# Kernel tuning notes

Measured on AMD Instinct MI355X. Metric: run time of the kernel, lower is better.

## Reference

```python
import jax, jax.numpy as jnp
import numpy as np
from jax import lax
from jax.scipy.stats import norm

K = 2            # top-k
NUM_EXPERTS = 4
NOISE_EPS = 0.01
LOSS_COEF = 0.01


def conv3x3(x, w):
    # x: [B,Cin,H,W], w: [Cout,Cin,3,3] -> [B,Cout,H,W]
    return lax.conv_general_dilated(x, w, (1, 1), 'SAME',
                                    dimension_numbers=('NCHW', 'OIHW', 'NCHW'))


def setup_inputs() -> dict:
    key = jax.random.key(0)
    ks = jax.random.split(key, 16)
    B, C, H, W = 16, 3, 256, 256
    FC = 2 * C                      # freq channels = 6
    HID = 64
    D = H * W * C                   # flattened gating dim = 196608
    f32 = jnp.float32
    inp = {
        'x':   jax.random.normal(ks[0], (B, C, H, W), f32),
        'ref': jax.random.normal(ks[1], (B, C, H, W), f32),
        'noise': jax.random.normal(ks[2], (B, NUM_EXPERTS), f32),
        'mod_w1': (jax.random.normal(ks[3], (FC, 2 * FC), f32) * 0.1),
        'mod_b1': jnp.zeros((FC,), f32),
        'mod_w2': (jax.random.normal(ks[4], (FC, FC), f32) * 0.1),
        'mod_b2': jnp.zeros((FC,), f32),
        'enh_w': (jax.random.normal(ks[5], (FC, FC), f32) * 0.1),
        'enh_b': jnp.zeros((FC,), f32),
        'fre_prompt': (jax.random.normal(ks[6], (FC, H, W // 2 + 1), f32) * 0.1),
        'w_gate':  (jax.random.normal(ks[7], (D, NUM_EXPERTS), f32) * 0.002),
        'w_noise': (jax.random.normal(ks[8], (D, NUM_EXPERTS), f32) * 0.002),
        'ew1': (jax.random.normal(ks[9],  (NUM_EXPERTS, HID, C, 3, 3), f32) * 0.05),
        'eb1': jnp.zeros((NUM_EXPERTS, HID), f32),
        'ew2': (jax.random.normal(ks[10], (NUM_EXPERTS, 1, HID, 3, 3), f32) * 0.05),
        'eb2': jnp.zeros((NUM_EXPERTS, 1), f32),
    }
    return inp


def _cv_squared(v):
    # torch .var() is unbiased (ddof=1)
    return jnp.var(v, ddof=1) / (jnp.mean(v) ** 2 + 1e-10)


def _forward(x, ref, noise, mod_w1, mod_b1, mod_w2, mod_b2, enh_w, enh_b,
             fre_prompt, w_gate, w_noise, ew1, eb1, ew2, eb2):
    B, C, H, W = x.shape

    # ---- frequency_prompt(ref) ----
    fft = jnp.fft.rfft2(ref, norm='ortho')                    # [B,C,H,W//2+1]
    freq = jnp.concatenate([fft.real, fft.imag], axis=1)      # [B,2C,H,Wf]
    # Adaptive avg/max pool to (H, W//2+1) are identities at native size
    pooled = jnp.concatenate([freq, freq], axis=1)            # [B,4C,H,Wf]
    m = jnp.einsum('oi,bihw->bohw', mod_w1, pooled) + mod_b1[:, None, None]
    m = jax.nn.relu(m)
    m = jnp.einsum('oi,bihw->bohw', mod_w2, m) + mod_b2[:, None, None]
    enh = m * fre_prompt[None]                                # [B,2C,H,Wf]
    enh = jax.nn.relu(jnp.einsum('oi,bihw->bohw', enh_w, enh) + enh_b[:, None, None])
    re, im = jnp.split(enh, 2, axis=1)
    spatial = jnp.fft.irfft2(re + 1j * im, s=(H, W), norm='ortho')  # [B,C,H,W]
    prompt = jax.nn.softmax(spatial.mean(axis=(2, 3), keepdims=True), axis=1)  # [B,C,1,1]

    # ---- noisy top-k gating ----
    x_ds = (x * prompt + x).reshape(B, -1)                    # [B, H*W*C]
    clean_logits = x_ds @ w_gate                              # [B,E]
    noise_stddev = jax.nn.softplus(x_ds @ w_noise) + NOISE_EPS
    noisy_logits = clean_logits + noise * noise_stddev
    top_vals, top_idx = lax.top_k(noisy_logits, K + 1)        # sorted desc, [B,K+1]
    tk_gates = jax.nn.softmax(top_vals[:, :K], axis=1)        # [B,K]
    gates = jnp.zeros_like(noisy_logits).at[
        jnp.arange(B)[:, None], top_idx[:, :K]].set(tk_gates)  # [B,E]

    # load = prob each expert's noisy logit lands in top-k
    thr_in = top_vals[:, K:K + 1]
    thr_out = top_vals[:, K - 1:K]
    is_in = noisy_logits > thr_in
    prob = jnp.where(is_in,
                     norm.cdf((clean_logits - thr_in) / noise_stddev),
                     norm.cdf((clean_logits - thr_out) / noise_stddev))
    load = prob.sum(0)
    importance = gates.sum(0)
    loss = (_cv_squared(importance) + _cv_squared(load)) * LOSS_COEF

    # ---- expert dispatch/combine (== weighted sum; gates are 0 off top-k) ----
    y = jnp.zeros((B, ew2.shape[1], H, W), x.dtype)
    for e in range(NUM_EXPERTS):
        h = jax.nn.relu(conv3x3(x, ew1[e]) + eb1[e][None, :, None, None])
        o = conv3x3(h, ew2[e]) + eb2[e][None, :, None, None]
        y = y + gates[:, e][:, None, None, None] * o
    return y, loss


def reference(x, ref, noise, mod_w1, mod_b1, mod_w2, mod_b2, enh_w, enh_b,
              fre_prompt, w_gate, w_noise, ew1, eb1, ew2, eb2):
    return _forward(x, ref, noise, mod_w1, mod_b1, mod_w2, mod_b2, enh_w, enh_b,
                    fre_prompt, w_gate, w_noise, ew1, eb1, ew2, eb2)
```

## Files before the change

kernel.cpp:

```cpp
#include <hip/hip_runtime.h>
#include <hip/hip_bf16.h>
#include <math.h>

#define WS_GATE 192
#define WS_GNP  256
#define WS_W1F  25088
#define WS_W2F  29184

typedef float    float4v __attribute__((ext_vector_type(4)));
typedef short    short8v __attribute__((ext_vector_type(8)));
typedef _Float16 half8v  __attribute__((ext_vector_type(8)));

union Q4 { uint4 q; short8v s; half8v h; };

__device__ __forceinline__ unsigned short bf16b(float f) {
    unsigned u = __builtin_bit_cast(unsigned, f);
    u = (u + 0x7FFFu + ((u >> 16) & 1u)) >> 16;
    return (unsigned short)u;
}

__device__ __forceinline__ unsigned pkbf16(float a, float b) {
#if __has_builtin(__builtin_amdgcn_cvt_pk_bf16_f32)
    return __builtin_bit_cast(unsigned, __builtin_amdgcn_cvt_pk_bf16_f32(a, b));
#else
    return (unsigned)bf16b(a) | ((unsigned)bf16b(b) << 16);
#endif
}

__device__ __forceinline__ unsigned pkf16(float a, float b) {
#if __has_builtin(__builtin_amdgcn_cvt_pkrtz)
    return __builtin_bit_cast(unsigned, __builtin_amdgcn_cvt_pkrtz(a, b));
#else
    union { _Float16 h[2]; unsigned u; } p;
    p.h[0] = (_Float16)a; p.h[1] = (_Float16)b;
    return p.u;
#endif
}

__global__ void k_aux(const float* __restrict__ ref, const float* __restrict__ x,
                      const float* __restrict__ wg,  const float* __restrict__ wn,
                      const float* __restrict__ ew1, const float* __restrict__ ew2,
                      float* __restrict__ ws) {
    __shared__ float sh[4][16][8];
    int blk = blockIdx.x, t = threadIdx.x;

    if (blk < 192) {
        int bc = blk >> 2, chunk = blk & 3;
        const float4* p4 = (const float4*)(ref + (size_t)bc*65536 + (size_t)chunk*16384);
        float acc = 0.f;
        #pragma unroll
        for (int i = 0; i < 16; ++i) { float4 v = p4[i*256 + t]; acc += v.x + v.y + v.z + v.w; }
        #pragma unroll
        for (int m = 1; m <= 32; m <<= 1) acc += __shfl_xor(acc, m);
        if ((t & 63) == 0) sh[0][0][t >> 6] = acc;
        __syncthreads();
        if (t == 0) ws[bc*4 + chunk] = sh[0][0][0] + sh[0][0][1] + sh[0][0][2] + sh[0][0][3];
        return;
    }
    if (blk < 384) {
        int r = blk - 192;
        int c = r >> 6, chunk = r & 63;
        int lane = t & 63, wv = t >> 6;
        int hw0 = chunk*1024 + t*4;
        const float4* wg4 = (const float4*)wg;
        const float4* wn4 = (const float4*)wn;
        const float4* x4  = (const float4*)x;
        float4 G[4], Nw[4];
        #pragma unroll
        for (int i = 0; i < 4; ++i) {
            G[i]  = wg4[c*65536 + hw0 + i];
            Nw[i] = wn4[c*65536 + hw0 + i];
        }
        for (int b = 0; b < 16; ++b) {
            float4 xv = x4[(b*3 + c)*16384 + chunk*256 + t];
            float xs[4] = {xv.x, xv.y, xv.z, xv.w};
            float aG[4] = {0,0,0,0}, aN[4] = {0,0,0,0};
            #pragma unroll
            for (int i = 0; i < 4; ++i) {
                aG[0] += xs[i]*G[i].x;  aG[1] += xs[i]*G[i].y;
                aG[2] += xs[i]*G[i].z;  aG[3] += xs[i]*G[i].w;
                aN[0] += xs[i]*Nw[i].x; aN[1] += xs[i]*Nw[i].y;
                aN[2] += xs[i]*Nw[i].z; aN[3] += xs[i]*Nw[i].w;
            }
            #pragma unroll
            for (int m = 1; m <= 32; m <<= 1) {
                #pragma unroll
                for (int e = 0; e < 4; ++e) {
                    aG[e] += __shfl_xor(aG[e], m);
                    aN[e] += __shfl_xor(aN[e], m);
                }
            }
            if (lane == 0) {
                #pragma unroll
                for (int e = 0; e < 4; ++e) { sh[wv][b][e] = aG[e]; sh[wv][b][4+e] = aN[e]; }
            }
        }
        __syncthreads();
        if (t < 128) {
            int b = t >> 3, s = t & 7;
            float v = sh[0][b][s] + sh[1][b][s] + sh[2][b][s] + sh[3][b][s];
            ws[WS_GNP + ((size_t)(c*64 + chunk)*16 + b)*8 + s] = v;
        }
        return;
    }
    uint4* w1f = (uint4*)(ws + WS_W1F);
    for (int i = t; i < 1024; i += 256) {
        int mm = i & 15, r = i >> 4, qq = r & 3, r2 = r >> 2, f = r2 & 3, e = r2 >> 2;
        const float* w1 = ew1 + e*1728 + (f*16 + mm)*27 + qq*8;
        int navail = 27 - qq*8;
        float v[8];
        #pragma unroll
        for (int j = 0; j < 8; ++j) v[j] = (j < navail) ? w1[j] : 0.f;
        uint4 q;
        q.x = pkbf16(v[0], v[1]); q.y = pkbf16(v[2], v[3]);
        q.z = pkbf16(v[4], v[5]); q.w = pkbf16(v[6], v[7]);
        w1f[i] = q;
    }
    uint4* w2f = (uint4*)(ws + WS_W2F);
    for (int i = t; i < 512; i += 256) {
        int qq = i & 3, r = i >> 2, ks = r & 1, r2 = r >> 1, mm = r2 & 15, e = r2 >> 4;
        uint4 q = make_uint4(0, 0, 0, 0);
        if (mm < 9) {
            float v[8];
            #pragma unroll
            for (int j = 0; j < 8; ++j) v[j] = ew2[e*576 + (ks*32 + qq*8 + j)*9 + mm];
            q.x = pkf16(v[0], v[1]); q.y = pkf16(v[2], v[3]);
            q.z = pkf16(v[4], v[5]); q.w = pkf16(v[6], v[7]);
        }
        w2f[i] = q;
    }
}

__global__ void k_gating(const float* __restrict__ noise,
                         const float* __restrict__ mw1, const float* __restrict__ mb1,
                         const float* __restrict__ mw2, const float* __restrict__ mb2,
                         const float* __restrict__ enw, const float* __restrict__ enb,
                         const float* __restrict__ fp,
                         float* __restrict__ ws, float* __restrict__ out) {
    __shared__ float GN2[48*8];
    __shared__ float gL[16][4], pL[16][4], cvs[2];
    int t = threadIdx.x;
    #pragma unroll
    for (int u = 0; u < 3; ++u) {
        int idx = t*3 + u;
        int bc = idx >> 3, s = idx & 7;
        int b = bc / 3, c = bc - b*3;
        float v = 0.f;
        for (int ch = 0; ch < 64; ++ch)
            v += ws[WS_GNP + ((size_t)(c*64 + ch)*16 + b)*8 + s];
        GN2[bc*8 + s] = v;
    }
    __syncthreads();
    if (t < 16) {
        int b = t;
        float sc[3];
        for (int c = 0; c < 3; ++c) {
            int bc = b*3 + c;
            sc[c] = (ws[bc*4] + ws[bc*4+1] + ws[bc*4+2] + ws[bc*4+3]) * (1.f/256.f);
        }
        float pooled[12];
        for (int i = 0; i < 12; ++i) { int r = i % 6; pooled[i] = (r < 3) ? sc[r] : 0.f; }
        float m1[6];
        for (int o = 0; o < 6; ++o) {
            float a = mb1[o];
            for (int i = 0; i < 12; ++i) a += mw1[o*12 + i] * pooled[i];
            m1[o] = fmaxf(a, 0.f);
        }
        float m2[6];
        for (int o = 0; o < 6; ++o) {
            float a = mb2[o];
            for (int i = 0; i < 6; ++i) a += mw2[o*6 + i] * m1[i];
            m2[o] = a * fp[(size_t)o * 33024];
        }
        float dc[3];
        for (int o = 0; o < 3; ++o) {
            float a = enb[o];
            for (int i = 0; i < 6; ++i) a += enw[o*6 + i] * m2[i];
            dc[o] = fmaxf(a, 0.f) * (1.f/256.f);
        }
        float mx = fmaxf(dc[0], fmaxf(dc[1], dc[2]));
        float e0 = expf(dc[0]-mx), e1 = expf(dc[1]-mx), e2 = expf(dc[2]-mx);
        float inv = 1.f / (e0 + e1 + e2);
        float pc[3] = { e0*inv + 1.f, e1*inv + 1.f, e2*inv + 1.f };
        float cl[4], sg[4], nz[4];
        for (int e = 0; e < 4; ++e) {
            float a = 0.f, nr = 0.f;
            for (int c = 0; c < 3; ++c) {
                a  += pc[c] * GN2[(b*3 + c)*8 + e];
                nr += pc[c] * GN2[(b*3 + c)*8 + 4 + e];
            }
            cl[e] = a;
            float sp = (nr > 20.f) ? nr : log1pf(expf(nr));
            sg[e] = sp + 0.01f;
            nz[e] = a + noise[b*4 + e] * sg[e];
        }
        int i0 = 0; float v0 = nz[0];
        for (int e = 1; e < 4; ++e) if (nz[e] > v0) { v0 = nz[e]; i0 = e; }
        int i1 = -1; float v1 = -3.4e38f;
        for (int e = 0; e < 4; ++e) if (e != i0 && nz[e] > v1) { v1 = nz[e]; i1 = e; }
        float v2 = -3.4e38f;
        for (int e = 0; e < 4; ++e) if (e != i0 && e != i1 && nz[e] > v2) v2 = nz[e];
        float ex = expf(v1 - v0), den = 1.f + ex;
        float gate[4] = {0.f, 0.f, 0.f, 0.f};
        gate[i0] = 1.f/den; gate[i1] = ex/den;
        for (int e = 0; e < 4; ++e) {
            ws[WS_GATE + b*4 + e] = gate[e];
            gL[b][e] = gate[e];
            float thr = (nz[e] > v2) ? v2 : v1;
            pL[b][e] = 0.5f * (1.f + erff((cl[e] - thr) / sg[e] * 0.70710678118f));
        }
    }
    __syncthreads();
    if (t < 2) {
        float v[4];
        for (int e = 0; e < 4; ++e) {
            float s = 0.f;
            for (int b = 0; b < 16; ++b) s += (t == 0) ? gL[b][e] : pL[b][e];
            v[e] = s;
        }
        float mean = 0.25f * (v[0] + v[1] + v[2] + v[3]);
        float var = 0.f;
        for (int e = 0; e < 4; ++e) { float d = v[e] - mean; var += d*d; }
        var *= (1.f/3.f);
        cvs[t] = var / (mean*mean + 1e-10f);
    }
    __syncthreads();
    if (t == 0) out[1048576] = (cvs[0] + cvs[1]) * 0.01f;
}

__global__ __launch_bounds__(256, 3)
void k_experts(const float* __restrict__ x,  const float* __restrict__ eb1,
               const float* __restrict__ eb2, const float* __restrict__ ws,
               float* __restrict__ out) {
    __shared__ __align__(16) uint4 s_hid[324*8];
    __shared__ __align__(16) char  s_mix[5904];
    float*    in_s = (float*)s_mix;
    _Float16* s_T  = (_Float16*)s_mix;

    int t = threadIdx.x;
    int b = blockIdx.x >> 8, tile = blockIdx.x & 255;
    int ty0 = (tile >> 4) * 16, tx0 = (tile & 15) * 16;
    const float* xb = x + (size_t)b * 196608;

    for (int i = t; i < 1200; i += 256) {
        int ci = i / 400, r = i - ci*400, iy = r / 20, ix = r - iy*20;
        int gy = ty0 - 2 + iy, gx = tx0 - 2 + ix;
        float v = 0.f;
        if ((unsigned)gy < 256u && (unsigned)gx < 256u) v = xb[ci*65536 + gy*256 + gx];
        in_s[i] = v;
    }
    __syncthreads();

    int lane = t & 63, wv = t >> 6;
    int qq = lane >> 4, mm = lane & 15;
    int oy = t >> 4, ox = t & 15;

    int offj[8];
    #pragma unroll
    for (int j = 0; j < 8; ++j) {
        int k = qq*8 + j;
        if (k < 27) { int ci = k/9, r = k - ci*9, kh = r/3, kw = r - kh*3;
                      offj[j] = ci*400 + kh*20 + kw; }
        else offj[j] = -1;
    }

    Q4 bfr[6];
    #pragma unroll
    for (int i = 0; i < 6; ++i) {
        int gidx = wv + i*4;
        if (gidx >= 21) break;
        int p = gidx*16 + mm;
        int py = p/18, px = p - py*18;
        int base = (p < 324) ? (py*20 + px) : 0;
        float v[8];
        #pragma unroll
        for (int j = 0; j < 8; ++j)
            v[j] = (offj[j] >= 0) ? in_s[base + offj[j]] : 0.f;
        bfr[i].q.x = pkbf16(v[0], v[1]); bfr[i].q.y = pkbf16(v[2], v[3]);
        bfr[i].q.z = pkbf16(v[4], v[5]); bfr[i].q.w = pkbf16(v[6], v[7]);
    }

    bool interior = (ty0 > 0) && (ty0 < 240) && (tx0 > 0) && (tx0 < 240);
    const float4 gates = *(const float4*)(ws + WS_GATE + b*4);
    float gv[4] = {gates.x, gates.y, gates.z, gates.w};
    const uint4* w1f = (const uint4*)(ws + WS_W1F);
    const uint4* w2f = (const uint4*)(ws + WS_W2F);
    float accY = 0.f;

    for (int e = 0; e < 4; ++e) {
        float g = gv[e];
        if (g == 0.f) continue;

        Q4 bw0, bw1;
        bw0.q = w2f[((e*16 + mm)*2 + 0)*4 + qq];
        bw1.q = w2f[((e*16 + mm)*2 + 1)*4 + qq];

        Q4 af[4];
        float4v cinit[4];
        #pragma unroll
        for (int f = 0; f < 4; ++f) {
            af[f].q = w1f[((e*4 + f)*4 + qq)*16 + mm];
            float4 bb = *(const float4*)(eb1 + e*64 + f*16 + qq*4);
            cinit[f] = (float4v){bb.x, bb.y, bb.z, bb.w};
        }

        #pragma unroll
        for (int i = 0; i < 6; ++i) {
            int gidx = wv + i*4;
            if (gidx >= 21) break;
            int p = gidx*16 + mm;
            bool valid = p < 324;
            float msk = 1.f;
            if (!interior) {
                int py = p/18, px = p - py*18;
                int gy = ty0 - 1 + py, gx = tx0 - 1 + px;
                msk = (((unsigned)gy < 256u) && ((unsigned)gx < 256u)) ? 1.f : 0.f;
            }
            #pragma unroll
            for (int f = 0; f < 4; ++f) {
                float4v d = __builtin_amdgcn_mfma_f32_16x16x32_bf16(
                    af[f].s, bfr[i].s, cinit[f], 0, 0, 0);
                if (valid) {
                    float h0 = fmaxf(d[0], 0.f);
                    float h1 = fmaxf(d[1], 0.f);
                    float h2 = fmaxf(d[2], 0.f);
                    float h3 = fmaxf(d[3], 0.f);
                    if (!interior) { h0 *= msk; h1 *= msk; h2 *= msk; h3 *= msk; }
                    uint2 pk = make_uint2(pkf16(h0, h1), pkf16(h2, h3));
                    int ch0 = f*16 + qq*4;
                    int hchunk = ch0 >> 3, hsel = (ch0 >> 2) & 1;
                    ((uint2*)&s_hid[p*8 + ((hchunk + p) & 7)])[hsel] = pk;
                }
            }
        }
        __syncthreads();

        for (int gi = wv; gi < 21; gi += 4) {
            int base = gi*16; if (base > 308) base = 308;
            int p = base + mm;
            Q4 a0, a1;
            a0.q = s_hid[p*8 + ((qq + p) & 7)];
            a1.q = s_hid[p*8 + ((4 + qq + p) & 7)];
            float4v d = __builtin_amdgcn_mfma_f32_16x16x32_f16(
                a0.h, bw0.h, (float4v){0.f,0.f,0.f,0.f}, 0, 0, 0);
            d = __builtin_amdgcn_mfma_f32_16x16x32_f16(a1.h, bw1.h, d, 0, 0, 0);
            if (mm < 9) {
                *(uint2*)&s_T[mm*328 + base + qq*4] =
                    make_uint2(pkf16(d[0], d[1]), pkf16(d[2], d[3]));
            }
        }
        __syncthreads();

        float oacc = 0.f;
        #pragma unroll
        for (int kh = 0; kh < 3; ++kh) {
            #pragma unroll
            for (int kw = 0; kw < 3; ++kw)
                oacc += (float)s_T[(kh*3 + kw)*328 + (oy + kh)*18 + ox + kw];
        }
        accY += g * (oacc + eb2[e]);
    }
    out[(size_t)b*65536 + (ty0 + oy)*256 + tx0 + ox] = accY;
}

extern "C" void kernel_launch(void* const* d_in, const int* in_sizes, int n_in,
                              void* d_out, int out_size, void* d_ws, size_t ws_size,
                              hipStream_t stream) {
    (void)in_sizes; (void)n_in; (void)out_size; (void)ws_size;
    const float* x     = (const float*)d_in[0];
    const float* ref   = (const float*)d_in[1];
    const float* noise = (const float*)d_in[2];
    const float* mw1   = (const float*)d_in[3];
    const float* mb1   = (const float*)d_in[4];
    const float* mw2   = (const float*)d_in[5];
    const float* mb2   = (const float*)d_in[6];
    const float* enw   = (const float*)d_in[7];
    const float* enb   = (const float*)d_in[8];
    const float* fp    = (const float*)d_in[9];
    const float* wg    = (const float*)d_in[10];
    const float* wn    = (const float*)d_in[11];
    const float* ew1   = (const float*)d_in[12];
    const float* eb1   = (const float*)d_in[13];
    const float* ew2   = (const float*)d_in[14];
    const float* eb2   = (const float*)d_in[15];
    float* out = (float*)d_out;
    float* ws  = (float*)d_ws;

    k_aux    <<<385, 256, 0, stream>>>(ref, x, wg, wn, ew1, ew2, ws);
    k_gating <<<1, 128, 0, stream>>>(noise, mw1, mb1, mw2, mb2, enw, enb, fp, ws, out);
    k_experts<<<4096, 256, 0, stream>>>(x, eb1, eb2, ws, out);
}
```

Baseline: 187.7 us.

## Fold gating into aux kernel via flag spin-wait; keep expert partials in fp32

Removes the separate single-block gating kernel launch by having the last k_aux block spin on per-block release flags and then run the gating logic itself. Separately, the expert kernel stores second-conv partial sums in fp32 shared memory instead of fp16 and adds the first-layer bias after the MFMA instead of using it as the accumulator init. The shared-memory buffer doubles in size, which may cut occupancy. The flags are never reset between calls, so on later calls the spin-wait may read stale flags and pass early.

After: 192.0 us. 2.3% more time.

```diff
diff --git a/kernel.cpp b/kernel.cpp
--- a/kernel.cpp
+++ b/kernel.cpp
@@ -6,6 +6,7 @@
 #define WS_GNP  256
 #define WS_W1F  25088
 #define WS_W2F  29184
+#define WS_FLAG 31232
 
 typedef float    float4v __attribute__((ext_vector_type(4)));
 typedef short    short8v __attribute__((ext_vector_type(8)));
@@ -40,9 +41,15 @@
 __global__ void k_aux(const float* __restrict__ ref, const float* __restrict__ x,
                       const float* __restrict__ wg,  const float* __restrict__ wn,
                       const float* __restrict__ ew1, const float* __restrict__ ew2,
-                      float* __restrict__ ws) {
+                      const float* __restrict__ noise,
+                      const float* __restrict__ mw1, const float* __restrict__ mb1,
+                      const float* __restrict__ mw2, const float* __restrict__ mb2,
+                      const float* __restrict__ enw, const float* __restrict__ enb,
+                      const float* __restrict__ fp,
+                      float* __restrict__ ws, float* __restrict__ out) {
     __shared__ float sh[4][16][8];
     int blk = blockIdx.x, t = threadIdx.x;
+    int* flags = (int*)(ws + WS_FLAG);
 
     if (blk < 192) {
         int bc = blk >> 2, chunk = blk & 3;
@@ -54,7 +61,10 @@
         for (int m = 1; m <= 32; m <<= 1) acc += __shfl_xor(acc, m);
         if ((t & 63) == 0) sh[0][0][t >> 6] = acc;
         __syncthreads();
-        if (t == 0) ws[bc*4 + chunk] = sh[0][0][0] + sh[0][0][1] + sh[0][0][2] + sh[0][0][3];
+        if (t == 0) {
+            ws[bc*4 + chunk] = sh[0][0][0] + sh[0][0][1] + sh[0][0][2] + sh[0][0][3];
+            __hip_atomic_store(flags + blk, 1, __ATOMIC_RELEASE, __HIP_MEMORY_SCOPE_AGENT);
+        }
         return;
     }
     if (blk < 384) {
@@ -101,8 +111,12 @@
             float v = sh[0][b][s] + sh[1][b][s] + sh[2][b][s] + sh[3][b][s];
             ws[WS_GNP + ((size_t)(c*64 + chunk)*16 + b)*8 + s] = v;
         }
+        __syncthreads();
+        if (t == 0)
+            __hip_atomic_store(flags + blk, 1, __ATOMIC_RELEASE, __HIP_MEMORY_SCOPE_AGENT);
         return;
     }
+
     uint4* w1f = (uint4*)(ws + WS_W1F);
     for (int i = t; i < 1024; i += 256) {
         int mm = i & 15, r = i >> 4, qq = r & 3, r2 = r >> 2, f = r2 & 3, e = r2 >> 2;
@@ -129,26 +143,30 @@
         }
         w2f[i] = q;
     }
-}
-
-__global__ void k_gating(const float* __restrict__ noise,
-                         const float* __restrict__ mw1, const float* __restrict__ mb1,
-                         const float* __restrict__ mw2, const float* __restrict__ mb2,
-                         const float* __restrict__ enw, const float* __restrict__ enb,
-                         const float* __restrict__ fp,
-                         float* __restrict__ ws, float* __restrict__ out) {
+
+    if (t < 128) {
+        #pragma unroll 1
+        for (int u = 0; u < 3; ++u) {
+            const int* f = flags + t*3 + u;
+            while (__hip_atomic_load(f, __ATOMIC_ACQUIRE, __HIP_MEMORY_SCOPE_AGENT) != 1)
+                __builtin_amdgcn_s_sleep(1);
+        }
+    }
+    __syncthreads();
+
     __shared__ float GN2[48*8];
     __shared__ float gL[16][4], pL[16][4], cvs[2];
-    int t = threadIdx.x;
-    #pragma unroll
-    for (int u = 0; u < 3; ++u) {
-        int idx = t*3 + u;
-        int bc = idx >> 3, s = idx & 7;
-        int b = bc / 3, c = bc - b*3;
-        float v = 0.f;
-        for (int ch = 0; ch < 64; ++ch)
-            v += ws[WS_GNP + ((size_t)(c*64 + ch)*16 + b)*8 + s];
-        GN2[bc*8 + s] = v;
+    if (t < 128) {
+        #pragma unroll
+        for (int u = 0; u < 3; ++u) {
+            int idx = t*3 + u;
+            int bc = idx >> 3, s = idx & 7;
+            int b = bc / 3, c = bc - b*3;
+            float v = 0.f;
+            for (int ch = 0; ch < 64; ++ch)
+                v += ws[WS_GNP + ((size_t)(c*64 + ch)*16 + b)*8 + s];
+            GN2[bc*8 + s] = v;
+        }
     }
     __syncthreads();
     if (t < 16) {
@@ -233,9 +251,9 @@
                const float* __restrict__ eb2, const float* __restrict__ ws,
                float* __restrict__ out) {
     __shared__ __align__(16) uint4 s_hid[324*8];
-    __shared__ __align__(16) char  s_mix[5904];
-    float*    in_s = (float*)s_mix;
-    _Float16* s_T  = (_Float16*)s_mix;
+    __shared__ __align__(16) char  s_mix[11808];
+    float* in_s = (float*)s_mix;
+    float* s_T  = (float*)s_mix;
 
     int t = threadIdx.x;
     int b = blockIdx.x >> 8, tile = blockIdx.x & 255;
@@ -296,12 +314,11 @@
         bw1.q = w2f[((e*16 + mm)*2 + 1)*4 + qq];
 
         Q4 af[4];
-        float4v cinit[4];
+        float4 bias[4];
         #pragma unroll
         for (int f = 0; f < 4; ++f) {
             af[f].q = w1f[((e*4 + f)*4 + qq)*16 + mm];
-            float4 bb = *(const float4*)(eb1 + e*64 + f*16 + qq*4);
-            cinit[f] = (float4v){bb.x, bb.y, bb.z, bb.w};
+            bias[f] = *(const float4*)(eb1 + e*64 + f*16 + qq*4);
         }
 
         #pragma unroll
@@ -319,12 +336,12 @@
             #pragma unroll
             for (int f = 0; f < 4; ++f) {
                 float4v d = __builtin_amdgcn_mfma_f32_16x16x32_bf16(
-                    af[f].s, bfr[i].s, cinit[f], 0, 0, 0);
+                    af[f].s, bfr[i].s, (float4v){0.f,0.f,0.f,0.f}, 0, 0, 0);
                 if (valid) {
-                    float h0 = fmaxf(d[0], 0.f);
-                    float h1 = fmaxf(d[1], 0.f);
-                    float h2 = fmaxf(d[2], 0.f);
-                    float h3 = fmaxf(d[3], 0.f);
+                    float h0 = fmaxf(d[0] + bias[f].x, 0.f);
+                    float h1 = fmaxf(d[1] + bias[f].y, 0.f);
+                    float h2 = fmaxf(d[2] + bias[f].z, 0.f);
+                    float h3 = fmaxf(d[3] + bias[f].w, 0.f);
                     if (!interior) { h0 *= msk; h1 *= msk; h2 *= msk; h3 *= msk; }
                     uint2 pk = make_uint2(pkf16(h0, h1), pkf16(h2, h3));
                     int ch0 = f*16 + qq*4;
@@ -345,8 +362,8 @@
                 a0.h, bw0.h, (float4v){0.f,0.f,0.f,0.f}, 0, 0, 0);
             d = __builtin_amdgcn_mfma_f32_16x16x32_f16(a1.h, bw1.h, d, 0, 0, 0);
             if (mm < 9) {
-                *(uint2*)&s_T[mm*328 + base + qq*4] =
-                    make_uint2(pkf16(d[0], d[1]), pkf16(d[2], d[3]));
+                float4* dst = (float4*)&s_T[mm*328 + base + qq*4];
+                *dst = make_float4(d[0], d[1], d[2], d[3]);
             }
         }
         __syncthreads();
@@ -356,7 +373,7 @@
         for (int kh = 0; kh < 3; ++kh) {
             #pragma unroll
             for (int kw = 0; kw < 3; ++kw)
-                oacc += (float)s_T[(kh*3 + kw)*328 + (oy + kh)*18 + ox + kw];
+                oacc += s_T[(kh*3 + kw)*328 + (oy + kh)*18 + ox + kw];
         }
         accY += g * (oacc + eb2[e]);
     }
@@ -386,7 +403,8 @@
     float* out = (float*)d_out;
     float* ws  = (float*)d_ws;
 
-    k_aux    <<<385, 256, 0, stream>>>(ref, x, wg, wn, ew1, ew2, ws);
-    k_gating <<<1, 128, 0, stream>>>(noise, mw1, mb1, mw2, mb2, enw, enb, fp, ws, out);
+    k_aux    <<<385, 256, 0, stream>>>(ref, x, wg, wn, ew1, ew2,
+                                       noise, mw1, mb1, mw2, mb2, enw, enb, fp,
+                                       ws, out);
     k_experts<<<4096, 256, 0, stream>>>(x, eb1, eb2, ws, out);
 }
```
